# Kernel tuning notes

Measured on AMD Instinct MI355X. Metric: run time of the kernel, lower is better.

## Reference

```python
import jax, jax.numpy as jnp
import numpy as np

N, B, H, OUT, T = 200000, 1024, 256, 128, 2  # nodes, graphs, hidden(=in_dim), out_dim, timesteps
NEG_SLOPE = 0.01


def setup_inputs() -> dict:
    key = jax.random.key(0)
    ks = jax.random.split(key, 12)
    s = 0.05
    f32 = jnp.float32
    return {
        "x": jax.random.normal(ks[0], (N, H), dtype=f32),
        "batch": jnp.sort(jax.random.randint(ks[1], (N,), 0, B)),
        # GATConv params (heads=1, shared lin for src/dst since in_channels is int)
        "W": jax.random.normal(ks[2], (H, H), dtype=f32) * s,
        "att_src": jax.random.normal(ks[3], (H,), dtype=f32) * s,
        "att_dst": jax.random.normal(ks[4], (H,), dtype=f32) * s,
        "bias_gat": jnp.zeros((H,), dtype=f32),
        # GRUCell params (input_size = H, hidden_size = H)
        "W_ih": jax.random.normal(ks[5], (3 * H, H), dtype=f32) * s,
        "W_hh": jax.random.normal(ks[6], (3 * H, H), dtype=f32) * s,
        "b_ih": jnp.zeros((3 * H,), dtype=f32),
        "b_hh": jnp.zeros((3 * H,), dtype=f32),
        # final Linear
        "W_lin": jax.random.normal(ks[7], (H, OUT), dtype=f32) * s,
        "b_lin": jnp.zeros((OUT,), dtype=f32),
    }


def reference(x, batch, W, att_src, att_dst, bias_gat, W_ih, W_hh, b_ih, b_hh, W_lin, b_lin):
    # out = global_add_pool(x, batch)  -> [B, H]
    out = jax.ops.segment_sum(x, batch, num_segments=B)
    for _ in range(T):
        # --- bipartite GATConv((x, out), edge_index=[arange(N), batch]) ---
        xs = x @ W                       # [N, H] transformed source nodes
        od = out @ W                     # [B, H] transformed dst (graph) nodes
        a_src = xs @ att_src             # [N]
        a_dst = od @ att_dst             # [B]
        e = a_src + a_dst[batch]         # [N] per-edge raw score (one edge per node)
        e = jnp.where(e > 0, e, NEG_SLOPE * e)  # leaky_relu(negative_slope=0.01)
        # scatter-softmax over each graph's incoming edges
        emax = jax.ops.segment_max(e, batch, num_segments=B)
        ee = jnp.exp(e - emax[batch])
        denom = jax.ops.segment_sum(ee, batch, num_segments=B)
        alpha = ee / denom[batch]        # [N]
        # scatter-add aggregation of weighted messages
        agg = jax.ops.segment_sum(xs * alpha[:, None], batch, num_segments=B) + bias_gat
        h = jax.nn.elu(agg)              # [B, H]  (dropout is identity in eval)
        # --- GRUCell(h, out) ---
        gi = h @ W_ih.T + b_ih           # [B, 3H]
        gh = out @ W_hh.T + b_hh         # [B, 3H]
        r = jax.nn.sigmoid(gi[:, :H] + gh[:, :H])
        z = jax.nn.sigmoid(gi[:, H:2 * H] + gh[:, H:2 * H])
        n = jnp.tanh(gi[:, 2 * H:] + r * gh[:, 2 * H:])
        out = jax.nn.silu((1.0 - z) * n + z * out)  # activation = F.silu
    return out @ W_lin + b_lin           # [B, OUT]
```

## Files before the change

kernel.cpp:

```cpp
#include <hip/hip_runtime.h>
#include <math.h>

#define N_NODES 200000
#define BGRAPH  1024
#define HDIM    256
#define ODIM    128
#define TSTEPS  2

__global__ __launch_bounds__(256) void k_prep(const float* __restrict__ W,
        const float* __restrict__ att_src, const float* __restrict__ att_dst,
        const int* __restrict__ batch, float* __restrict__ v, float* __restrict__ u,
        int* __restrict__ seg) {
    int t = threadIdx.x;
    if (blockIdx.x < 256) {
        int i = blockIdx.x;
        float w = W[(size_t)i * HDIM + t];
        __shared__ float r1[256], r2[256];
        r1[t] = w * att_src[t];
        r2[t] = w * att_dst[t];
        __syncthreads();
        for (int st = 128; st > 0; st >>= 1) {
            if (t < st) { r1[t] += r1[t + st]; r2[t] += r2[t + st]; }
            __syncthreads();
        }
        if (t == 0) { v[i] = r1[0]; u[i] = r2[0]; }
    } else {
        int b = (blockIdx.x - 256) * 256 + t;
        if (b > BGRAPH) return;
        if (b == BGRAPH) { seg[b] = N_NODES; return; }
        int lo = 0, hi = N_NODES;
        while (lo < hi) { int mid = (lo + hi) >> 1; if (batch[mid] < b) lo = mid + 1; else hi = mid; }
        seg[b] = lo;
    }
}

__global__ __launch_bounds__(256) void k_passA(const float* __restrict__ x,
        const int* __restrict__ seg, const float* __restrict__ v,
        float* __restrict__ stt, float* __restrict__ smax) {
    int b = blockIdx.x;
    int lo = seg[b], hi = seg[b + 1];
    int t = threadIdx.x, wave = t >> 6, lane = t & 63;
    float v0 = v[4 * lane + 0], v1 = v[4 * lane + 1], v2 = v[4 * lane + 2], v3 = v[4 * lane + 3];
    float p0 = 0.f, p1 = 0.f, p2 = 0.f, p3 = 0.f;
    float sm = -3.402823466e38f;
    int i = lo + wave;
    for (; i + 12 < hi; i += 16) {
        const float4 r0 = *(const float4*)(x + (size_t)i * HDIM + 4 * lane);
        const float4 r1 = *(const float4*)(x + (size_t)(i + 4) * HDIM + 4 * lane);
        const float4 r2 = *(const float4*)(x + (size_t)(i + 8) * HDIM + 4 * lane);
        const float4 r3 = *(const float4*)(x + (size_t)(i + 12) * HDIM + 4 * lane);
        p0 += r0.x + r1.x + r2.x + r3.x; p1 += r0.y + r1.y + r2.y + r3.y;
        p2 += r0.z + r1.z + r2.z + r3.z; p3 += r0.w + r1.w + r2.w + r3.w;
        float d0 = r0.x * v0 + r0.y * v1 + r0.z * v2 + r0.w * v3;
        float d1 = r1.x * v0 + r1.y * v1 + r1.z * v2 + r1.w * v3;
        float d2 = r2.x * v0 + r2.y * v1 + r2.z * v2 + r2.w * v3;
        float d3 = r3.x * v0 + r3.y * v1 + r3.z * v2 + r3.w * v3;
        #pragma unroll
        for (int off = 1; off < 64; off <<= 1) {
            d0 += __shfl_xor(d0, off, 64);
            d1 += __shfl_xor(d1, off, 64);
            d2 += __shfl_xor(d2, off, 64);
            d3 += __shfl_xor(d3, off, 64);
        }
        sm = fmaxf(sm, fmaxf(fmaxf(d0, d1), fmaxf(d2, d3)));
    }
    for (; i < hi; i += 4) {
        const float4 r0 = *(const float4*)(x + (size_t)i * HDIM + 4 * lane);
        p0 += r0.x; p1 += r0.y; p2 += r0.z; p3 += r0.w;
        float d0 = r0.x * v0 + r0.y * v1 + r0.z * v2 + r0.w * v3;
        #pragma unroll
        for (int off = 1; off < 64; off <<= 1) d0 += __shfl_xor(d0, off, 64);
        sm = fmaxf(sm, d0);
    }
    __shared__ float comb[4][HDIM];
    comb[wave][4 * lane + 0] = p0; comb[wave][4 * lane + 1] = p1;
    comb[wave][4 * lane + 2] = p2; comb[wave][4 * lane + 3] = p3;
    __shared__ float sred[4];
    if (lane == 0) sred[wave] = sm;
    __syncthreads();
    stt[(size_t)b * HDIM + t] = comb[0][t] + comb[1][t] + comb[2][t] + comb[3][t];
    if (t == 0) smax[b] = fmaxf(fmaxf(sred[0], sred[1]), fmaxf(sred[2], sred[3]));
}

template<int DO_GRU>
__global__ __launch_bounds__(256) void k_iter_h(const float* __restrict__ x,
        const int* __restrict__ seg, const float* __restrict__ v,
        const float* __restrict__ u, const float* __restrict__ smax,
        float* __restrict__ stt,
        const float* __restrict__ gi, const float* __restrict__ gh,
        const float* __restrict__ b_ih, const float* __restrict__ b_hh,
        const float* __restrict__ W, const float* __restrict__ bias_gat,
        float* __restrict__ hbuf) {
    int b = blockIdx.x, t = threadIdx.x;
    int lo = seg[b], hi = seg[b + 1];
    float st_j;
    if (DO_GRU) {
        size_t base = (size_t)b * (3 * HDIM);
        float gir = gi[base + t] + b_ih[t];
        float giz = gi[base + HDIM + t] + b_ih[HDIM + t];
        float gin = gi[base + 2 * HDIM + t] + b_ih[2 * HDIM + t];
        float ghr = gh[base + t] + b_hh[t];
        float ghz = gh[base + HDIM + t] + b_hh[HDIM + t];
        float ghn = gh[base + 2 * HDIM + t] + b_hh[2 * HDIM + t];
        float r = 1.f / (1.f + __expf(-(gir + ghr)));
        float z = 1.f / (1.f + __expf(-(giz + ghz)));
        float n = tanhf(gin + r * ghn);
        float prev = stt[(size_t)b * HDIM + t];
        float h2 = (1.f - z) * n + z * prev;
        st_j = h2 / (1.f + __expf(-h2));
        stt[(size_t)b * HDIM + t] = st_j;
    } else {
        st_j = stt[(size_t)b * HDIM + t];
    }
    __shared__ float red[256];
    red[t] = st_j * u[t];
    __syncthreads();
    for (int st = 128; st > 0; st >>= 1) { if (t < st) red[t] += red[t + st]; __syncthreads(); }
    float datt = red[0];
    __syncthreads();
    float M = smax[b] + datt;
    M = M > 0.f ? M : 0.01f * M;

    int wave = t >> 6, lane = t & 63;
    float v0 = v[4 * lane + 0], v1 = v[4 * lane + 1], v2 = v[4 * lane + 2], v3 = v[4 * lane + 3];
    float a0 = 0.f, a1 = 0.f, a2 = 0.f, a3 = 0.f, den = 0.f;
    int i = lo + wave;
    for (; i + 12 < hi; i += 16) {
        const float4 r0 = *(const float4*)(x + (size_t)i * HDIM + 4 * lane);
        const float4 r1 = *(const float4*)(x + (size_t)(i + 4) * HDIM + 4 * lane);
        const float4 r2 = *(const float4*)(x + (size_t)(i + 8) * HDIM + 4 * lane);
        const float4 r3 = *(const float4*)(x + (size_t)(i + 12) * HDIM + 4 * lane);
        float d0 = r0.x * v0 + r0.y * v1 + r0.z * v2 + r0.w * v3;
        float d1 = r1.x * v0 + r1.y * v1 + r1.z * v2 + r1.w * v3;
        float d2 = r2.x * v0 + r2.y * v1 + r2.z * v2 + r2.w * v3;
        float d3 = r3.x * v0 + r3.y * v1 + r3.z * v2 + r3.w * v3;
        #pragma unroll
        for (int off = 1; off < 64; off <<= 1) {
            d0 += __shfl_xor(d0, off, 64);
            d1 += __shfl_xor(d1, off, 64);
            d2 += __shfl_xor(d2, off, 64);
            d3 += __shfl_xor(d3, off, 64);
        }
        float e0 = d0 + datt; e0 = e0 > 0.f ? e0 : 0.01f * e0;
        float e1 = d1 + datt; e1 = e1 > 0.f ? e1 : 0.01f * e1;
        float e2 = d2 + datt; e2 = e2 > 0.f ? e2 : 0.01f * e2;
        float e3 = d3 + datt; e3 = e3 > 0.f ? e3 : 0.01f * e3;
        float w0 = __expf(e0 - M), w1 = __expf(e1 - M);
        float w2 = __expf(e2 - M), w3 = __expf(e3 - M);
        den += (w0 + w1) + (w2 + w3);
        a0 += w0 * r0.x + w1 * r1.x + w2 * r2.x + w3 * r3.x;
        a1 += w0 * r0.y + w1 * r1.y + w2 * r2.y + w3 * r3.y;
        a2 += w0 * r0.z + w1 * r1.z + w2 * r2.z + w3 * r3.z;
        a3 += w0 * r0.w + w1 * r1.w + w2 * r2.w + w3 * r3.w;
    }
    for (; i < hi; i += 4) {
        const float4 r0 = *(const float4*)(x + (size_t)i * HDIM + 4 * lane);
        float d0 = r0.x * v0 + r0.y * v1 + r0.z * v2 + r0.w * v3;
        #pragma unroll
        for (int off = 1; off < 64; off <<= 1) d0 += __shfl_xor(d0, off, 64);
        float e0 = d0 + datt; e0 = e0 > 0.f ? e0 : 0.01f * e0;
        float w0 = __expf(e0 - M);
        den += w0;
        a0 += w0 * r0.x; a1 += w0 * r0.y; a2 += w0 * r0.z; a3 += w0 * r0.w;
    }
    __shared__ float comb[4][HDIM];
    __shared__ float dred[4];
    comb[wave][4 * lane + 0] = a0; comb[wave][4 * lane + 1] = a1;
    comb[wave][4 * lane + 2] = a2; comb[wave][4 * lane + 3] = a3;
    if (lane == 0) dred[wave] = den;
    __syncthreads();
    float dtot = dred[0] + dred[1] + dred[2] + dred[3];
    float inv = (hi > lo) ? 1.0f / dtot : 0.f;
    __shared__ float ax[HDIM];
    ax[t] = (comb[0][t] + comb[1][t] + comb[2][t] + comb[3][t]) * inv;
    __syncthreads();
    float acc = bias_gat[t];
    #pragma unroll 8
    for (int ii = 0; ii < HDIM; ++ii) acc += ax[ii] * W[(size_t)ii * HDIM + t];
    hbuf[(size_t)b * HDIM + t] = acc > 0.f ? acc : expm1f(acc);
}

__global__ __launch_bounds__(256) void k_gemm2(const float* __restrict__ A0,
        const float* __restrict__ A1, const float* __restrict__ B0,
        const float* __restrict__ B1, float* __restrict__ C0, float* __restrict__ C1,
        int M, int N, int K) {
    const float* A = blockIdx.z ? A1 : A0;
    const float* B = blockIdx.z ? B1 : B0;
    float* C = blockIdx.z ? C1 : C0;
    __shared__ __align__(16) float As[16][64];
    __shared__ __align__(16) float Bs[16][64];
    int tx = threadIdx.x & 15, ty = threadIdx.x >> 4;
    int m0 = blockIdx.x * 64, n0 = blockIdx.y * 64;
    float acc[4][4] = {};
    for (int k0 = 0; k0 < K; k0 += 16) {
        {
            int r = threadIdx.x >> 2;
            int kk = (threadIdx.x & 3) << 2;
            float4 av = *(const float4*)(A + (size_t)(m0 + r) * K + k0 + kk);
            As[kk + 0][r] = av.x; As[kk + 1][r] = av.y;
            As[kk + 2][r] = av.z; As[kk + 3][r] = av.w;
            float4 bv = *(const float4*)(B + (size_t)(n0 + r) * K + k0 + kk);
            Bs[kk + 0][r] = bv.x; Bs[kk + 1][r] = bv.y;
            Bs[kk + 2][r] = bv.z; Bs[kk + 3][r] = bv.w;
        }
        __syncthreads();
        #pragma unroll
        for (int kk = 0; kk < 16; ++kk) {
            float4 a = *(const float4*)&As[kk][ty * 4];
            float4 bb = *(const float4*)&Bs[kk][tx * 4];
            acc[0][0] += a.x * bb.x; acc[0][1] += a.x * bb.y; acc[0][2] += a.x * bb.z; acc[0][3] += a.x * bb.w;
            acc[1][0] += a.y * bb.x; acc[1][1] += a.y * bb.y; acc[1][2] += a.y * bb.z; acc[1][3] += a.y * bb.w;
            acc[2][0] += a.z * bb.x; acc[2][1] += a.z * bb.y; acc[2][2] += a.z * bb.z; acc[2][3] += a.z * bb.w;
            acc[3][0] += a.w * bb.x; acc[3][1] += a.w * bb.y; acc[3][2] += a.w * bb.z; acc[3][3] += a.w * bb.w;
        }
        __syncthreads();
    }
    #pragma unroll
    for (int i = 0; i < 4; ++i) {
        int mrow = m0 + ty * 4 + i;
        *(float4*)(C + (size_t)mrow * N + n0 + tx * 4) =
            make_float4(acc[i][0], acc[i][1], acc[i][2], acc[i][3]);
    }
}

__global__ __launch_bounds__(256) void k_final(const float* __restrict__ gi,
        const float* __restrict__ gh, const float* __restrict__ b_ih,
        const float* __restrict__ b_hh, const float* __restrict__ stt,
        const float* __restrict__ B, const float* __restrict__ bias,
        float* __restrict__ C, int M, int N, int K) {
    __shared__ __align__(16) float As[16][64];
    __shared__ __align__(16) float Bs[16][64];
    int tx = threadIdx.x & 15, ty = threadIdx.x >> 4;
    int m0 = blockIdx.x * 64, n0 = blockIdx.y * 64;
    float acc[4][4] = {};
    for (int k0 = 0; k0 < K; k0 += 16) {
        {
            int r = threadIdx.x >> 2;
            int kk0 = (threadIdx.x & 3) << 2;
            int mrow = m0 + r;
            size_t base = (size_t)mrow * (3 * HDIM);
            #pragma unroll
            for (int q = 0; q < 4; ++q) {
                int k = k0 + kk0 + q;
                float gir = gi[base + k] + b_ih[k];
                float giz = gi[base + HDIM + k] + b_ih[HDIM + k];
                float gin = gi[base + 2 * HDIM + k] + b_ih[2 * HDIM + k];
                float ghr = gh[base + k] + b_hh[k];
                float ghz = gh[base + HDIM + k] + b_hh[HDIM + k];
                float ghn = gh[base + 2 * HDIM + k] + b_hh[2 * HDIM + k];
                float rg = 1.f / (1.f + __expf(-(gir + ghr)));
                float zg = 1.f / (1.f + __expf(-(giz + ghz)));
                float ng = tanhf(gin + rg * ghn);
                float prev = stt[(size_t)mrow * HDIM + k];
                float h2 = (1.f - zg) * ng + zg * prev;
                As[kk0 + q][r] = h2 / (1.f + __expf(-h2));
            }
        }
        {
            int kk = threadIdx.x >> 4;
            int nn = (threadIdx.x & 15) << 2;
            float4 bv = *(const float4*)(B + (size_t)(k0 + kk) * N + n0 + nn);
            Bs[kk][nn + 0] = bv.x; Bs[kk][nn + 1] = bv.y;
            Bs[kk][nn + 2] = bv.z; Bs[kk][nn + 3] = bv.w;
        }
        __syncthreads();
        #pragma unroll
        for (int kk = 0; kk < 16; ++kk) {
            float4 a = *(const float4*)&As[kk][ty * 4];
            float4 bb = *(const float4*)&Bs[kk][tx * 4];
            acc[0][0] += a.x * bb.x; acc[0][1] += a.x * bb.y; acc[0][2] += a.x * bb.z; acc[0][3] += a.x * bb.w;
            acc[1][0] += a.y * bb.x; acc[1][1] += a.y * bb.y; acc[1][2] += a.y * bb.z; acc[1][3] += a.y * bb.w;
            acc[2][0] += a.z * bb.x; acc[2][1] += a.z * bb.y; acc[2][2] += a.z * bb.z; acc[2][3] += a.z * bb.w;
            acc[3][0] += a.w * bb.x; acc[3][1] += a.w * bb.y; acc[3][2] += a.w * bb.z; acc[3][3] += a.w * bb.w;
        }
        __syncthreads();
    }
    float bsv[4];
    #pragma unroll
    for (int j = 0; j < 4; ++j) bsv[j] = bias[n0 + tx * 4 + j];
    #pragma unroll
    for (int i = 0; i < 4; ++i) {
        int mrow = m0 + ty * 4 + i;
        *(float4*)(C + (size_t)mrow * N + n0 + tx * 4) =
            make_float4(acc[i][0] + bsv[0], acc[i][1] + bsv[1],
                        acc[i][2] + bsv[2], acc[i][3] + bsv[3]);
    }
}

extern "C" void kernel_launch(void* const* d_in, const int* in_sizes, int n_in,
                              void* d_out, int out_size, void* d_ws, size_t ws_size,
                              hipStream_t stream) {
    const float* x        = (const float*)d_in[0];
    const int*   batch    = (const int*)d_in[1];
    const float* W        = (const float*)d_in[2];
    const float* att_src  = (const float*)d_in[3];
    const float* att_dst  = (const float*)d_in[4];
    const float* bias_gat = (const float*)d_in[5];
    const float* W_ih     = (const float*)d_in[6];
    const float* W_hh     = (const float*)d_in[7];
    const float* b_ih     = (const float*)d_in[8];
    const float* b_hh     = (const float*)d_in[9];
    const float* W_lin    = (const float*)d_in[10];
    const float* b_lin    = (const float*)d_in[11];

    char* ws = (char*)d_ws;
    size_t off = 0;
    auto alloc = [&](size_t bytes) {
        void* p = (void*)(ws + off);
        off += (bytes + 255) & ~(size_t)255;
        return p;
    };
    int*   seg  = (int*)alloc((BGRAPH + 1) * 4);
    float* vv   = (float*)alloc(HDIM * 4);
    float* uu   = (float*)alloc(HDIM * 4);
    float* smax = (float*)alloc(BGRAPH * 4);
    float* stt  = (float*)alloc((size_t)BGRAPH * HDIM * 4);
    float* hbuf = (float*)alloc((size_t)BGRAPH * HDIM * 4);
    float* gi   = (float*)alloc((size_t)BGRAPH * 3 * HDIM * 4);
    float* gh   = (float*)alloc((size_t)BGRAPH * 3 * HDIM * 4);

    hipLaunchKernelGGL(k_prep, dim3(261), dim3(256), 0, stream,
                       W, att_src, att_dst, batch, vv, uu, seg);
    hipLaunchKernelGGL(k_passA, dim3(BGRAPH), dim3(256), 0, stream, x, seg, vv, stt, smax);

    hipLaunchKernelGGL((k_iter_h<0>), dim3(BGRAPH), dim3(256), 0, stream,
                       x, seg, vv, uu, smax, stt, (const float*)nullptr, (const float*)nullptr,
                       b_ih, b_hh, W, bias_gat, hbuf);
    hipLaunchKernelGGL(k_gemm2, dim3(BGRAPH / 64, (3 * HDIM) / 64, 2), dim3(256), 0,
                       stream, hbuf, stt, W_ih, W_hh, gi, gh, BGRAPH, 3 * HDIM, HDIM);
    hipLaunchKernelGGL((k_iter_h<1>), dim3(BGRAPH), dim3(256), 0, stream,
                       x, seg, vv, uu, smax, stt, gi, gh,
                       b_ih, b_hh, W, bias_gat, hbuf);
    hipLaunchKernelGGL(k_gemm2, dim3(BGRAPH / 64, (3 * HDIM) / 64, 2), dim3(256), 0,
                       stream, hbuf, stt, W_ih, W_hh, gi, gh, BGRAPH, 3 * HDIM, HDIM);
    hipLaunchKernelGGL(k_final, dim3(BGRAPH / 64, ODIM / 64), dim3(256), 0, stream,
                       gi, gh, b_ih, b_hh, stt, W_lin, b_lin, (float*)d_out,
                       BGRAPH, ODIM, HDIM);
}
```

Before: 518.0 us.

## Fuse pooling with first attention step and cache per-node scores

Merges the pooling pass and the first GAT iteration into one kernel, so x is read twice in one block (the second read is likely cache-resident) rather than in two separate launches. Per-node source attention scores are computed once, stored in a global buffer (and in shared memory when a graph's segment fits in SCAP), and reused in both iterations. This removes the dot products and wave shuffle reductions from the iteration loops. The unroll depth drops from 4 rows to 2 rows per wave, and an extra N-sized workspace buffer is needed.

```diff
diff --git a/kernel.cpp b/kernel.cpp
--- a/kernel.cpp
+++ b/kernel.cpp
@@ -5,7 +5,7 @@
 #define BGRAPH  1024
 #define HDIM    256
 #define ODIM    128
-#define TSTEPS  2
+#define SCAP    1024
 
 __global__ __launch_bounds__(256) void k_prep(const float* __restrict__ W,
         const float* __restrict__ att_src, const float* __restrict__ att_dst,
@@ -34,57 +34,110 @@
     }
 }
 
-__global__ __launch_bounds__(256) void k_passA(const float* __restrict__ x,
+__global__ __launch_bounds__(256) void k_passAB(const float* __restrict__ x,
         const int* __restrict__ seg, const float* __restrict__ v,
-        float* __restrict__ stt, float* __restrict__ smax) {
+        const float* __restrict__ u, const float* __restrict__ W,
+        const float* __restrict__ bias_gat,
+        float* __restrict__ s, float* __restrict__ smax,
+        float* __restrict__ stt, float* __restrict__ hbuf) {
     int b = blockIdx.x;
     int lo = seg[b], hi = seg[b + 1];
     int t = threadIdx.x, wave = t >> 6, lane = t & 63;
     float v0 = v[4 * lane + 0], v1 = v[4 * lane + 1], v2 = v[4 * lane + 2], v3 = v[4 * lane + 3];
+    __shared__ float s_loc[SCAP];
+    __shared__ float comb[4][HDIM];
+    __shared__ float red[256];
+    __shared__ float sred[4], dred[4];
+    bool inl = (hi - lo) <= SCAP;
+
     float p0 = 0.f, p1 = 0.f, p2 = 0.f, p3 = 0.f;
     float sm = -3.402823466e38f;
     int i = lo + wave;
-    for (; i + 12 < hi; i += 16) {
+    for (; i + 4 < hi; i += 8) {
         const float4 r0 = *(const float4*)(x + (size_t)i * HDIM + 4 * lane);
         const float4 r1 = *(const float4*)(x + (size_t)(i + 4) * HDIM + 4 * lane);
-        const float4 r2 = *(const float4*)(x + (size_t)(i + 8) * HDIM + 4 * lane);
-        const float4 r3 = *(const float4*)(x + (size_t)(i + 12) * HDIM + 4 * lane);
-        p0 += r0.x + r1.x + r2.x + r3.x; p1 += r0.y + r1.y + r2.y + r3.y;
-        p2 += r0.z + r1.z + r2.z + r3.z; p3 += r0.w + r1.w + r2.w + r3.w;
-        float d0 = r0.x * v0 + r0.y * v1 + r0.z * v2 + r0.w * v3;
-        float d1 = r1.x * v0 + r1.y * v1 + r1.z * v2 + r1.w * v3;
-        float d2 = r2.x * v0 + r2.y * v1 + r2.z * v2 + r2.w * v3;
-        float d3 = r3.x * v0 + r3.y * v1 + r3.z * v2 + r3.w * v3;
+        p0 += r0.x + r1.x; p1 += r0.y + r1.y; p2 += r0.z + r1.z; p3 += r0.w + r1.w;
+        float pa = r0.x * v0 + r0.y * v1 + r0.z * v2 + r0.w * v3;
+        float pb = r1.x * v0 + r1.y * v1 + r1.z * v2 + r1.w * v3;
         #pragma unroll
-        for (int off = 1; off < 64; off <<= 1) {
-            d0 += __shfl_xor(d0, off, 64);
-            d1 += __shfl_xor(d1, off, 64);
-            d2 += __shfl_xor(d2, off, 64);
-            d3 += __shfl_xor(d3, off, 64);
-        }
-        sm = fmaxf(sm, fmaxf(fmaxf(d0, d1), fmaxf(d2, d3)));
+        for (int off = 32; off > 0; off >>= 1) {
+            pa += __shfl_down(pa, off, 64);
+            pb += __shfl_down(pb, off, 64);
+        }
+        if (lane == 0) {
+            s[i] = pa; s[i + 4] = pb;
+            if (inl) { s_loc[i - lo] = pa; s_loc[i + 4 - lo] = pb; }
+            sm = fmaxf(sm, fmaxf(pa, pb));
+        }
     }
     for (; i < hi; i += 4) {
         const float4 r0 = *(const float4*)(x + (size_t)i * HDIM + 4 * lane);
         p0 += r0.x; p1 += r0.y; p2 += r0.z; p3 += r0.w;
-        float d0 = r0.x * v0 + r0.y * v1 + r0.z * v2 + r0.w * v3;
+        float pa = r0.x * v0 + r0.y * v1 + r0.z * v2 + r0.w * v3;
         #pragma unroll
-        for (int off = 1; off < 64; off <<= 1) d0 += __shfl_xor(d0, off, 64);
-        sm = fmaxf(sm, d0);
-    }
-    __shared__ float comb[4][HDIM];
+        for (int off = 32; off > 0; off >>= 1) pa += __shfl_down(pa, off, 64);
+        if (lane == 0) {
+            s[i] = pa;
+            if (inl) s_loc[i - lo] = pa;
+            sm = fmaxf(sm, pa);
+        }
+    }
     comb[wave][4 * lane + 0] = p0; comb[wave][4 * lane + 1] = p1;
     comb[wave][4 * lane + 2] = p2; comb[wave][4 * lane + 3] = p3;
-    __shared__ float sred[4];
     if (lane == 0) sred[wave] = sm;
     __syncthreads();
-    stt[(size_t)b * HDIM + t] = comb[0][t] + comb[1][t] + comb[2][t] + comb[3][t];
-    if (t == 0) smax[b] = fmaxf(fmaxf(sred[0], sred[1]), fmaxf(sred[2], sred[3]));
-}
-
-template<int DO_GRU>
-__global__ __launch_bounds__(256) void k_iter_h(const float* __restrict__ x,
-        const int* __restrict__ seg, const float* __restrict__ v,
+    float st0 = comb[0][t] + comb[1][t] + comb[2][t] + comb[3][t];
+    stt[(size_t)b * HDIM + t] = st0;
+    float smx = fmaxf(fmaxf(sred[0], sred[1]), fmaxf(sred[2], sred[3]));
+    if (t == 0) smax[b] = smx;
+    red[t] = st0 * u[t];
+    __syncthreads();
+    for (int st = 128; st > 0; st >>= 1) { if (t < st) red[t] += red[t + st]; __syncthreads(); }
+    float d1 = red[0];
+    __syncthreads();
+    float M = smx + d1;
+    M = M > 0.f ? M : 0.01f * M;
+
+    float a0 = 0.f, a1 = 0.f, a2 = 0.f, a3 = 0.f, den = 0.f;
+    i = lo + wave;
+    for (; i + 4 < hi; i += 8) {
+        float s0v = inl ? s_loc[i - lo]     : s[i];
+        float s1v = inl ? s_loc[i + 4 - lo] : s[i + 4];
+        float e0 = s0v + d1; e0 = e0 > 0.f ? e0 : 0.01f * e0;
+        float e1 = s1v + d1; e1 = e1 > 0.f ? e1 : 0.01f * e1;
+        float w0 = __expf(e0 - M), w1 = __expf(e1 - M);
+        const float4 r0 = *(const float4*)(x + (size_t)i * HDIM + 4 * lane);
+        const float4 r1 = *(const float4*)(x + (size_t)(i + 4) * HDIM + 4 * lane);
+        den += w0 + w1;
+        a0 += w0 * r0.x + w1 * r1.x; a1 += w0 * r0.y + w1 * r1.y;
+        a2 += w0 * r0.z + w1 * r1.z; a3 += w0 * r0.w + w1 * r1.w;
+    }
+    for (; i < hi; i += 4) {
+        float s0v = inl ? s_loc[i - lo] : s[i];
+        float e0 = s0v + d1; e0 = e0 > 0.f ? e0 : 0.01f * e0;
+        float w0 = __expf(e0 - M);
+        const float4 r0 = *(const float4*)(x + (size_t)i * HDIM + 4 * lane);
+        den += w0;
+        a0 += w0 * r0.x; a1 += w0 * r0.y; a2 += w0 * r0.z; a3 += w0 * r0.w;
+    }
+    __syncthreads();
+    comb[wave][4 * lane + 0] = a0; comb[wave][4 * lane + 1] = a1;
+    comb[wave][4 * lane + 2] = a2; comb[wave][4 * lane + 3] = a3;
+    if (lane == 0) dred[wave] = den;
+    __syncthreads();
+    float dtot = dred[0] + dred[1] + dred[2] + dred[3];
+    float inv = (hi > lo) ? 1.0f / dtot : 0.f;
+    __shared__ float ax[HDIM];
+    ax[t] = (comb[0][t] + comb[1][t] + comb[2][t] + comb[3][t]) * inv;
+    __syncthreads();
+    float acc = bias_gat[t];
+    #pragma unroll 8
+    for (int ii = 0; ii < HDIM; ++ii) acc += ax[ii] * W[(size_t)ii * HDIM + t];
+    hbuf[(size_t)b * HDIM + t] = acc > 0.f ? acc : expm1f(acc);
+}
+
+__global__ __launch_bounds__(256) void k_iter2(const float* __restrict__ x,
+        const int* __restrict__ seg, const float* __restrict__ s,
         const float* __restrict__ u, const float* __restrict__ smax,
         float* __restrict__ stt,
         const float* __restrict__ gi, const float* __restrict__ gh,
@@ -93,73 +146,47 @@
         float* __restrict__ hbuf) {
     int b = blockIdx.x, t = threadIdx.x;
     int lo = seg[b], hi = seg[b + 1];
-    float st_j;
-    if (DO_GRU) {
-        size_t base = (size_t)b * (3 * HDIM);
-        float gir = gi[base + t] + b_ih[t];
-        float giz = gi[base + HDIM + t] + b_ih[HDIM + t];
-        float gin = gi[base + 2 * HDIM + t] + b_ih[2 * HDIM + t];
-        float ghr = gh[base + t] + b_hh[t];
-        float ghz = gh[base + HDIM + t] + b_hh[HDIM + t];
-        float ghn = gh[base + 2 * HDIM + t] + b_hh[2 * HDIM + t];
-        float r = 1.f / (1.f + __expf(-(gir + ghr)));
-        float z = 1.f / (1.f + __expf(-(giz + ghz)));
-        float n = tanhf(gin + r * ghn);
-        float prev = stt[(size_t)b * HDIM + t];
-        float h2 = (1.f - z) * n + z * prev;
-        st_j = h2 / (1.f + __expf(-h2));
-        stt[(size_t)b * HDIM + t] = st_j;
-    } else {
-        st_j = stt[(size_t)b * HDIM + t];
-    }
+    size_t base = (size_t)b * (3 * HDIM);
+    float gir = gi[base + t] + b_ih[t];
+    float giz = gi[base + HDIM + t] + b_ih[HDIM + t];
+    float gin = gi[base + 2 * HDIM + t] + b_ih[2 * HDIM + t];
+    float ghr = gh[base + t] + b_hh[t];
+    float ghz = gh[base + HDIM + t] + b_hh[HDIM + t];
+    float ghn = gh[base + 2 * HDIM + t] + b_hh[2 * HDIM + t];
+    float r = 1.f / (1.f + __expf(-(gir + ghr)));
+    float z = 1.f / (1.f + __expf(-(giz + ghz)));
+    float n = tanhf(gin + r * ghn);
+    float prev = stt[(size_t)b * HDIM + t];
+    float h2 = (1.f - z) * n + z * prev;
+    float st_j = h2 / (1.f + __expf(-h2));
+    stt[(size_t)b * HDIM + t] = st_j;
+
     __shared__ float red[256];
     red[t] = st_j * u[t];
     __syncthreads();
     for (int st = 128; st > 0; st >>= 1) { if (t < st) red[t] += red[t + st]; __syncthreads(); }
-    float datt = red[0];
-    __syncthreads();
-    float M = smax[b] + datt;
+    float d2 = red[0];
+    __syncthreads();
+    float M = smax[b] + d2;
     M = M > 0.f ? M : 0.01f * M;
 
     int wave = t >> 6, lane = t & 63;
-    float v0 = v[4 * lane + 0], v1 = v[4 * lane + 1], v2 = v[4 * lane + 2], v3 = v[4 * lane + 3];
     float a0 = 0.f, a1 = 0.f, a2 = 0.f, a3 = 0.f, den = 0.f;
     int i = lo + wave;
-    for (; i + 12 < hi; i += 16) {
+    for (; i + 4 < hi; i += 8) {
+        float e0 = s[i] + d2;     e0 = e0 > 0.f ? e0 : 0.01f * e0;
+        float e1 = s[i + 4] + d2; e1 = e1 > 0.f ? e1 : 0.01f * e1;
+        float w0 = __expf(e0 - M), w1 = __expf(e1 - M);
         const float4 r0 = *(const float4*)(x + (size_t)i * HDIM + 4 * lane);
         const float4 r1 = *(const float4*)(x + (size_t)(i + 4) * HDIM + 4 * lane);
-        const float4 r2 = *(const float4*)(x + (size_t)(i + 8) * HDIM + 4 * lane);
-        const float4 r3 = *(const float4*)(x + (size_t)(i + 12) * HDIM + 4 * lane);
-        float d0 = r0.x * v0 + r0.y * v1 + r0.z * v2 + r0.w * v3;
-        float d1 = r1.x * v0 + r1.y * v1 + r1.z * v2 + r1.w * v3;
-        float d2 = r2.x * v0 + r2.y * v1 + r2.z * v2 + r2.w * v3;
-        float d3 = r3.x * v0 + r3.y * v1 + r3.z * v2 + r3.w * v3;
-        #pragma unroll
-        for (int off = 1; off < 64; off <<= 1) {
-            d0 += __shfl_xor(d0, off, 64);
-            d1 += __shfl_xor(d1, off, 64);
-            d2 += __shfl_xor(d2, off, 64);
-            d3 += __shfl_xor(d3, off, 64);
-        }
-        float e0 = d0 + datt; e0 = e0 > 0.f ? e0 : 0.01f * e0;
-        float e1 = d1 + datt; e1 = e1 > 0.f ? e1 : 0.01f * e1;
-        float e2 = d2 + datt; e2 = e2 > 0.f ? e2 : 0.01f * e2;
-        float e3 = d3 + datt; e3 = e3 > 0.f ? e3 : 0.01f * e3;
-        float w0 = __expf(e0 - M), w1 = __expf(e1 - M);
-        float w2 = __expf(e2 - M), w3 = __expf(e3 - M);
-        den += (w0 + w1) + (w2 + w3);
-        a0 += w0 * r0.x + w1 * r1.x + w2 * r2.x + w3 * r3.x;
-        a1 += w0 * r0.y + w1 * r1.y + w2 * r2.y + w3 * r3.y;
-        a2 += w0 * r0.z + w1 * r1.z + w2 * r2.z + w3 * r3.z;
-        a3 += w0 * r0.w + w1 * r1.w + w2 * r2.w + w3 * r3.w;
+        den += w0 + w1;
+        a0 += w0 * r0.x + w1 * r1.x; a1 += w0 * r0.y + w1 * r1.y;
+        a2 += w0 * r0.z + w1 * r1.z; a3 += w0 * r0.w + w1 * r1.w;
     }
     for (; i < hi; i += 4) {
-        const float4 r0 = *(const float4*)(x + (size_t)i * HDIM + 4 * lane);
-        float d0 = r0.x * v0 + r0.y * v1 + r0.z * v2 + r0.w * v3;
-        #pragma unroll
-        for (int off = 1; off < 64; off <<= 1) d0 += __shfl_xor(d0, off, 64);
-        float e0 = d0 + datt; e0 = e0 > 0.f ? e0 : 0.01f * e0;
+        float e0 = s[i] + d2; e0 = e0 > 0.f ? e0 : 0.01f * e0;
         float w0 = __expf(e0 - M);
+        const float4 r0 = *(const float4*)(x + (size_t)i * HDIM + 4 * lane);
         den += w0;
         a0 += w0 * r0.x; a1 += w0 * r0.y; a2 += w0 * r0.z; a3 += w0 * r0.w;
     }
@@ -314,6 +341,7 @@
     float* vv   = (float*)alloc(HDIM * 4);
     float* uu   = (float*)alloc(HDIM * 4);
     float* smax = (float*)alloc(BGRAPH * 4);
+    float* s    = (float*)alloc((size_t)N_NODES * 4);
     float* stt  = (float*)alloc((size_t)BGRAPH * HDIM * 4);
     float* hbuf = (float*)alloc((size_t)BGRAPH * HDIM * 4);
     float* gi   = (float*)alloc((size_t)BGRAPH * 3 * HDIM * 4);
@@ -321,16 +349,12 @@
 
     hipLaunchKernelGGL(k_prep, dim3(261), dim3(256), 0, stream,
                        W, att_src, att_dst, batch, vv, uu, seg);
-    hipLaunchKernelGGL(k_passA, dim3(BGRAPH), dim3(256), 0, stream, x, seg, vv, stt, smax);
-
-    hipLaunchKernelGGL((k_iter_h<0>), dim3(BGRAPH), dim3(256), 0, stream,
-                       x, seg, vv, uu, smax, stt, (const float*)nullptr, (const float*)nullptr,
-                       b_ih, b_hh, W, bias_gat, hbuf);
+    hipLaunchKernelGGL(k_passAB, dim3(BGRAPH), dim3(256), 0, stream,
+                       x, seg, vv, uu, W, bias_gat, s, smax, stt, hbuf);
     hipLaunchKernelGGL(k_gemm2, dim3(BGRAPH / 64, (3 * HDIM) / 64, 2), dim3(256), 0,
                        stream, hbuf, stt, W_ih, W_hh, gi, gh, BGRAPH, 3 * HDIM, HDIM);
-    hipLaunchKernelGGL((k_iter_h<1>), dim3(BGRAPH), dim3(256), 0, stream,
-                       x, seg, vv, uu, smax, stt, gi, gh,
-                       b_ih, b_hh, W, bias_gat, hbuf);
+    hipLaunchKernelGGL(k_iter2, dim3(BGRAPH), dim3(256), 0, stream,
+                       x, seg, s, uu, smax, stt, gi, gh, b_ih, b_hh, W, bias_gat, hbuf);
     hipLaunchKernelGGL(k_gemm2, dim3(BGRAPH / 64, (3 * HDIM) / 64, 2), dim3(256), 0,
                        stream, hbuf, stt, W_ih, W_hh, gi, gh, BGRAPH, 3 * HDIM, HDIM);
     hipLaunchKernelGGL(k_final, dim3(BGRAPH / 64, ODIM / 64), dim3(256), 0, stream,
```

Measured after the change: 508.0 us. Within noise of the previous version (-1.9%).
